# Kernel tuning notes

Hardware: AMD Instinct MI355X
Metric: run time of the kernel (lower is better)

## Reference

```python
import jax, jax.numpy as jnp
import numpy as np

NS, NW, E, DIN, OUT, H = 100_000, 400_000, 500_000, 64, 64, 4


def setup_inputs() -> dict:
    key = jax.random.key(0)
    ks = jax.random.split(key, 26)
    s = 1.0 / np.sqrt(DIN)
    sg = 1.0 / np.sqrt(OUT)
    inp = {
        "x_sites": jax.random.normal(ks[0], (NS, DIN), jnp.float32),
        "x_wells": jax.random.normal(ks[1], (NW, DIN), jnp.float32),
        "edge_sw_src": jax.random.randint(ks[2], (E,), 0, NS, jnp.int32),
        "edge_sw_dst": jax.random.randint(ks[3], (E,), 0, NW, jnp.int32),
        "edge_ws_src": jax.random.randint(ks[4], (E,), 0, NW, jnp.int32),
        "edge_ws_dst": jax.random.randint(ks[5], (E,), 0, NS, jnp.int32),
        # GAT ('pfas_sites','distance','gw_wells'), heads=4, concat=False
        "W_sw": jax.random.normal(ks[6], (DIN, H * OUT), jnp.float32) * s,
        "att_src_sw": jax.random.normal(ks[7], (H, OUT), jnp.float32) * sg,
        "att_dst_sw": jax.random.normal(ks[8], (H, OUT), jnp.float32) * sg,
        "b_sw": jnp.zeros((OUT,), jnp.float32),
        # SAGE ('gw_wells','distance','pfas_sites')
        "Wl_ws": jax.random.normal(ks[9], (DIN, OUT), jnp.float32) * s,
        "bl_ws": jnp.zeros((OUT,), jnp.float32),
        "Wr_ws": jax.random.normal(ks[10], (DIN, OUT), jnp.float32) * s,
        # GAT ('pfas_sites','self_loop','pfas_sites'), add_self_loops=True -> identity edges
        "W_ss": jax.random.normal(ks[11], (DIN, H * OUT), jnp.float32) * s,
        "att_src_ss": jax.random.normal(ks[12], (H, OUT), jnp.float32) * sg,
        "att_dst_ss": jax.random.normal(ks[13], (H, OUT), jnp.float32) * sg,
        "b_ss": jnp.zeros((OUT,), jnp.float32),
        # SAGE ('gw_wells','self_loop','gw_wells') with identity edges
        "Wl_ww": jax.random.normal(ks[14], (DIN, OUT), jnp.float32) * s,
        "bl_ww": jnp.zeros((OUT,), jnp.float32),
        "Wr_ww": jax.random.normal(ks[15], (DIN, OUT), jnp.float32) * s,
        # output heads
        "Wg": jax.random.normal(ks[16], (OUT, 1), jnp.float32) * sg,
        "bg": jnp.zeros((1,), jnp.float32),
        "Wsit": jax.random.normal(ks[17], (OUT, 1), jnp.float32) * sg,
        "bsit": jnp.zeros((1,), jnp.float32),
    }
    return inp


def _gat(x_src, x_dst, src, dst, W, a_src, a_dst, b, n_dst):
    """PyG GATConv, concat=False (mean over heads), negative_slope=0.2."""
    h, c = a_src.shape
    xs = (x_src @ W).reshape(-1, h, c)  # [Ns,H,C]
    xd = (x_dst @ W).reshape(-1, h, c)  # [Nd,H,C]
    al_s = jnp.einsum("nhc,hc->nh", xs, a_src)
    al_d = jnp.einsum("nhc,hc->nh", xd, a_dst)
    e = jax.nn.leaky_relu(al_s[src] + al_d[dst], 0.2)  # [E,H]
    m = jax.ops.segment_max(e, dst, num_segments=n_dst)
    ex = jnp.exp(e - m[dst])
    denom = jax.ops.segment_sum(ex, dst, num_segments=n_dst)
    alpha = ex / denom[dst]  # edge-softmax per dst node
    msg = xs[src] * alpha[:, :, None]  # [E,H,C] dominant intermediate
    out = jax.ops.segment_sum(msg, dst, num_segments=n_dst)
    return out.mean(axis=1) + b


def _sage(x_src, x_dst, src, dst, Wl, bl, Wr, n_dst):
    """PyG SAGEConv, mean aggregation, root_weight=True."""
    ssum = jax.ops.segment_sum(x_src[src], dst, num_segments=n_dst)
    cnt = jax.ops.segment_sum(jnp.ones((src.shape[0],), x_src.dtype), dst, num_segments=n_dst)
    mean = ssum / jnp.maximum(cnt, 1.0)[:, None]  # empty neighborhood -> 0 (PyG mean scatter)
    return mean @ Wl + bl + x_dst @ Wr


def reference(x_sites, x_wells, edge_sw_src, edge_sw_dst, edge_ws_src, edge_ws_dst,
              W_sw, att_src_sw, att_dst_sw, b_sw, Wl_ws, bl_ws, Wr_ws,
              W_ss, att_src_ss, att_dst_ss, b_ss, Wl_ww, bl_ww, Wr_ww,
              Wg, bg, Wsit, bsit):
    # relation 1: GAT sites -> wells
    gw = _gat(x_sites, x_wells, edge_sw_src, edge_sw_dst, W_sw, att_src_sw, att_dst_sw, b_sw, NW)
    # relation 4: SAGE self-loop on wells; identity edges -> mean == x itself
    gw = gw + (x_wells @ Wl_ww + bl_ww + x_wells @ Wr_ww)  # HeteroConv aggr='sum'
    # relation 2: SAGE wells -> sites
    si = _sage(x_wells, x_sites, edge_ws_src, edge_ws_dst, Wl_ws, bl_ws, Wr_ws, NS)
    # relation 3: GAT self-loop on sites (add_self_loops=True -> identity edge set);
    # softmax over a single self edge is 1, so output = mean over heads of lin(x) + bias
    si = si + (x_sites @ W_ss).reshape(NS, H, OUT).mean(axis=1) + b_ss
    # post: relu -> dropout (eval mode: identity) -> linear -> leaky_relu(0.01)
    gw = jax.nn.relu(gw)
    si = jax.nn.relu(si)
    o_gw = jax.nn.leaky_relu(gw @ Wg + bg, 0.01)   # [NW, 1]
    o_si = jax.nn.leaky_relu(si @ Wsit + bsit, 0.01)  # [NS, 1]
    return o_gw, o_si
```

## Files before the change

### kernel.cpp

```cpp
#include <hip/hip_runtime.h>

#define NS_ 100000
#define NW_ 400000
#define NE_ 500000
#define EPB 2048

typedef float f32x4_t __attribute__((ext_vector_type(4)));
typedef unsigned u32x4_t __attribute__((ext_vector_type(4)));

__device__ __forceinline__ float lrelu02(float x) { return x > 0.f ? x : 0.2f * x; }
__device__ __forceinline__ float bf2f(unsigned short u) {
    return __uint_as_float(((unsigned)u) << 16);
}
__device__ __forceinline__ unsigned short f2bf(float f) {
    unsigned u = __float_as_uint(f);
    u += 0x7FFFu + ((u >> 16) & 1u);
    return (unsigned short)(u >> 16);
}
__device__ __forceinline__ unsigned pk(float lo, float hi) {
    return (unsigned)f2bf(lo) | ((unsigned)f2bf(hi) << 16);
}
__device__ __forceinline__ void mfma_bf16(f32x4_t& acc, u32x4_t a, u32x4_t b) {
    asm volatile("v_mfma_f32_16x16x32_bf16 %0, %1, %2, %0" : "+v"(acc) : "v"(a), "v"(b));
}

__global__ void __launch_bounds__(256)
k_prep(const float* __restrict__ W_sw, const float* __restrict__ att_src,
       const float* __restrict__ att_dst,
       const float* __restrict__ Wl_ww, const float* __restrict__ Wr_ww,
       const float* __restrict__ Wl_ws, const float* __restrict__ Wr_ws,
       const float* __restrict__ W_ss,
       float* __restrict__ vd, float* __restrict__ vs,
       u32x4_t* __restrict__ fw, u32x4_t* __restrict__ fs,
       u32x4_t* __restrict__ fsp)
{
    const int tid = threadIdx.x;
    {
        int d = tid >> 2, h = tid & 3;
        const float4* wp = (const float4*)(W_sw + d * 256 + h * 64);
        const float4* ad = (const float4*)(att_dst + h * 64);
        const float4* as = (const float4*)(att_src + h * 64);
        float accd = 0.f, accs = 0.f;
#pragma unroll
        for (int c = 0; c < 16; ++c) {
            float4 wv = wp[c]; float4 dv = ad[c]; float4 sv = as[c];
            accd += wv.x * dv.x + wv.y * dv.y + wv.z * dv.z + wv.w * dv.w;
            accs += wv.x * sv.x + wv.y * sv.y + wv.z * sv.z + wv.w * sv.w;
        }
        vd[d * 4 + h] = accd;
        vs[d * 4 + h] = accs;
    }
    for (int idx = tid; idx < 512; idx += 256) {
        int f = idx >> 6, lane = idx & 63;
        int kc = f >> 2, ct = f & 3, q = lane >> 4, n = lane & 15;
        int c = ct * 16 + n;
        u32x4_t d;
#pragma unroll
        for (int i = 0; i < 4; ++i) {
            int k = kc * 32 + q * 8 + 2 * i;
            d[i] = pk(Wl_ww[k * 64 + c] + Wr_ww[k * 64 + c],
                      Wl_ww[(k + 1) * 64 + c] + Wr_ww[(k + 1) * 64 + c]);
        }
        fw[idx] = d;
    }
    for (int idx = tid; idx < 1024; idx += 256) {
        int f = idx >> 6, lane = idx & 63;
        int kc = f >> 2, ct = f & 3, q = lane >> 4, n = lane & 15;
        int c = ct * 16 + n;
        u32x4_t d;
#pragma unroll
        for (int i = 0; i < 4; ++i) {
            int k = kc * 32 + q * 8 + 2 * i;
            float lo, hi;
            if (k < 64) {
                lo = Wl_ws[k * 64 + c];
                hi = Wl_ws[(k + 1) * 64 + c];
            } else {
                int kk = k - 64;
                lo = Wr_ws[kk * 64 + c] + 0.25f * (W_ss[kk * 256 + c] + W_ss[kk * 256 + 64 + c] +
                                                   W_ss[kk * 256 + 128 + c] + W_ss[kk * 256 + 192 + c]);
                hi = Wr_ws[(kk + 1) * 64 + c] + 0.25f * (W_ss[(kk + 1) * 256 + c] + W_ss[(kk + 1) * 256 + 64 + c] +
                                                         W_ss[(kk + 1) * 256 + 128 + c] + W_ss[(kk + 1) * 256 + 192 + c]);
            }
            d[i] = pk(lo, hi);
        }
        fs[idx] = d;
    }
    for (int idx = tid; idx < 2048; idx += 256) {
        int f = idx >> 6, lane = idx & 63;
        int kc = f >> 4, ct = f & 15, q = lane >> 4, n = lane & 15;
        int c = ct * 16 + n;
        u32x4_t d;
#pragma unroll
        for (int i = 0; i < 4; ++i) {
            int k = kc * 32 + q * 8 + 2 * i;
            d[i] = pk(W_sw[k * 256 + c], W_sw[(k + 1) * 256 + c]);
        }
        fsp[idx] = d;
    }
}

#define SP_PAD 264
__global__ void __launch_bounds__(256)
k_sites_pre(const float* __restrict__ x_sites, const u32x4_t* __restrict__ fsp,
            const float* __restrict__ vs, unsigned short* __restrict__ xs,
            float* __restrict__ al_s)
{
    __shared__ unsigned short stg[4][16 * SP_PAD];
    __shared__ float vsl[256];
    const int tid = threadIdx.x;
    vsl[tid] = vs[tid];
    __syncthreads();
    const int wave = __builtin_amdgcn_readfirstlane(tid >> 6);
    const int lane = tid & 63, q = lane >> 4, n = lane & 15;
    const int sbase = blockIdx.x * 64 + wave * 16;
    const int srow = min(sbase + n, NS_ - 1);
    const float* xr = x_sites + (size_t)srow * 64 + q * 8;
    float4 x0 = *(const float4*)(xr);
    float4 x1 = *(const float4*)(xr + 4);
    float4 x2 = *(const float4*)(xr + 32);
    float4 x3 = *(const float4*)(xr + 36);
    u32x4_t am0 = { pk(x0.x, x0.y), pk(x0.z, x0.w), pk(x1.x, x1.y), pk(x1.z, x1.w) };
    u32x4_t am1 = { pk(x2.x, x2.y), pk(x2.z, x2.w), pk(x3.x, x3.y), pk(x3.z, x3.w) };
    float pa[4];
#pragma unroll
    for (int h = 0; h < 4; ++h) {
        const float* v0 = &vsl[(q * 8) * 4 + h];
        const float* v1 = &vsl[(32 + q * 8) * 4 + h];
        pa[h] = x0.x * v0[0]  + x0.y * v0[4]  + x0.z * v0[8]  + x0.w * v0[12]
              + x1.x * v0[16] + x1.y * v0[20] + x1.z * v0[24] + x1.w * v0[28]
              + x2.x * v1[0]  + x2.y * v1[4]  + x2.z * v1[8]  + x2.w * v1[12]
              + x3.x * v1[16] + x3.y * v1[20] + x3.z * v1[24] + x3.w * v1[28];
    }
#pragma unroll
    for (int h = 0; h < 4; ++h) {
        pa[h] += __shfl_xor(pa[h], 16, 64);
        pa[h] += __shfl_xor(pa[h], 32, 64);
    }
    if (q == 0 && sbase + n < NS_)
        *(float4*)(al_s + (size_t)(sbase + n) * 4) = make_float4(pa[0], pa[1], pa[2], pa[3]);

    f32x4_t acc[16];
#pragma unroll
    for (int ct = 0; ct < 16; ++ct) acc[ct] = (f32x4_t){0, 0, 0, 0};
    asm volatile("s_nop 3" : "+v"(am0), "+v"(am1));
#pragma unroll
    for (int ct = 0; ct < 16; ++ct) mfma_bf16(acc[ct], am0, fsp[ct * 64 + lane]);
#pragma unroll
    for (int ct = 0; ct < 16; ++ct) mfma_bf16(acc[ct], am1, fsp[(16 + ct) * 64 + lane]);
    asm volatile("s_nop 7\n\ts_nop 7" ::: "memory");
    unsigned short* ss = &stg[wave][0];
#pragma unroll
    for (int ct = 0; ct < 16; ++ct)
#pragma unroll
        for (int reg = 0; reg < 4; ++reg)
            ss[(q * 4 + reg) * SP_PAD + ct * 16 + n] = f2bf(acc[ct][reg]);
    __builtin_amdgcn_s_waitcnt(0);
#pragma unroll
    for (int i = 0; i < 8; ++i) {
        int g = i * 64 + lane;
        int r = g >> 5, c = g & 31;
        if (sbase + r < NS_) {
            u32x4_t v = *(const u32x4_t*)(ss + r * SP_PAD + c * 8);
            *(u32x4_t*)(xs + (size_t)(sbase + r) * 256 + c * 8) = v;
        }
    }
}

__global__ void __launch_bounds__(256)
k_hist2(const int* __restrict__ d1, int* __restrict__ h1,
        const int* __restrict__ d2, int* __restrict__ h2)
{
    int e = blockIdx.x * 256 + threadIdx.x;
    if (e >= NE_) return;
    if (blockIdx.y == 0) atomicAdd(&h1[d1[e]], 1);
    else                 atomicAdd(&h2[d2[e]], 1);
}

__global__ void __launch_bounds__(256)
k_scan1_2(const int* __restrict__ h1, int n1, int* __restrict__ b1, int nb1,
          const int* __restrict__ h2, int n2, int* __restrict__ b2)
{
    __shared__ int red[256];
    const int tid = threadIdx.x;
    const int bx = blockIdx.x;
    const int* hist; int n; int* bsum; int blk;
    if (bx < nb1) { hist = h1; n = n1; bsum = b1; blk = bx; }
    else          { hist = h2; n = n2; bsum = b2; blk = bx - nb1; }
    int base = blk * EPB + tid * 8;
    int s = 0;
#pragma unroll
    for (int i = 0; i < 8; ++i) { int idx = base + i; if (idx < n) s += hist[idx]; }
    red[tid] = s;
    __syncthreads();
    for (int off = 128; off > 0; off >>= 1) {
        if (tid < off) red[tid] += red[tid + off];
        __syncthreads();
    }
    if (tid == 0) bsum[blk] = red[0];
}

__global__ void __launch_bounds__(256)
k_scan2_2(int* __restrict__ b1, int nb1, int* __restrict__ b2, int nb2)
{
    __shared__ int sh[256];
    const int tid = threadIdx.x;
    int* bsum = blockIdx.x == 0 ? b1 : b2;
    int nb = blockIdx.x == 0 ? nb1 : nb2;
    sh[tid] = (tid < nb) ? bsum[tid] : 0;
    __syncthreads();
    for (int off = 1; off < 256; off <<= 1) {
        int u = (tid >= off) ? sh[tid - off] : 0;
        __syncthreads();
        sh[tid] += u;
        __syncthreads();
    }
    if (tid < nb) bsum[tid] = (tid == 0) ? 0 : sh[tid - 1];
}

__global__ void __launch_bounds__(256)
k_scan3_2(const int* __restrict__ h1, int n1, const int* __restrict__ b1,
          int* __restrict__ rp1, int* __restrict__ cu1, int nb1,
          const int* __restrict__ h2, int n2, const int* __restrict__ b2,
          int* __restrict__ rp2, int* __restrict__ cu2)
{
    __shared__ int tsum[256];
    const int tid = threadIdx.x;
    const int bx = blockIdx.x;
    const int* hist; int n; const int* bsum; int* rowptr; int* cursor; int blk;
    if (bx < nb1) { hist = h1; n = n1; bsum = b1; rowptr = rp1; cursor = cu1; blk = bx; }
    else          { hist = h2; n = n2; bsum = b2; rowptr = rp2; cursor = cu2; blk = bx - nb1; }
    int base = blk * EPB + tid * 8;
    int v[8]; int s = 0;
#pragma unroll
    for (int i = 0; i < 8; ++i) {
        int idx = base + i;
        v[i] = (idx < n) ? hist[idx] : 0;
        s += v[i];
    }
    tsum[tid] = s;
    __syncthreads();
    for (int off = 1; off < 256; off <<= 1) {
        int u = (tid >= off) ? tsum[tid - off] : 0;
        __syncthreads();
        tsum[tid] += u;
        __syncthreads();
    }
    int texcl = tsum[tid] - s;
    int run = bsum[blk] + texcl;
#pragma unroll
    for (int i = 0; i < 8; ++i) {
        int idx = base + i;
        if (idx < n) { rowptr[idx] = run; cursor[idx] = run; run += v[i]; }
    }
    if (blk == 0 && tid == 0) rowptr[n] = NE_;
}

__global__ void __launch_bounds__(256)
k_scatter2(const int* __restrict__ s1, const int* __restrict__ d1,
           int* __restrict__ c1, int* __restrict__ o1,
           const int* __restrict__ s2, const int* __restrict__ d2,
           int* __restrict__ c2, int* __restrict__ o2)
{
    int e = blockIdx.x * 256 + threadIdx.x;
    if (e >= NE_) return;
    if (blockIdx.y == 0) { int p = atomicAdd(&c1[d1[e]], 1); o1[p] = s1[e]; }
    else                 { int p = atomicAdd(&c2[d2[e]], 1); o2[p] = s2[e]; }
}

__global__ void __launch_bounds__(256)
k_gat_gather(const float* __restrict__ x_wells, const float* __restrict__ vd,
             const int* __restrict__ rowptr, const int* __restrict__ csr_src,
             const float* __restrict__ al_s, const unsigned short* __restrict__ xs,
             const float* __restrict__ b_sw, const float* __restrict__ bl_ww,
             unsigned short* __restrict__ tg)
{
    __shared__ float vdl[256];
    __shared__ float biasl[64];
    const int tid = threadIdx.x;
    vdl[tid] = vd[tid];
    if (tid < 64) biasl[tid] = b_sw[tid] + bl_ww[tid];
    __syncthreads();
    const int wl = tid >> 4, p = tid & 15;
    const int w = blockIdx.x * 16 + wl;
    float h0, h1, h2, h3;
    {
        float4 xv = *(const float4*)(x_wells + (size_t)w * 64 + 4 * p);
        const float* vp = &vdl[16 * p];
        h0 = xv.x * vp[0] + xv.y * vp[4] + xv.z * vp[8]  + xv.w * vp[12];
        h1 = xv.x * vp[1] + xv.y * vp[5] + xv.z * vp[9]  + xv.w * vp[13];
        h2 = xv.x * vp[2] + xv.y * vp[6] + xv.z * vp[10] + xv.w * vp[14];
        h3 = xv.x * vp[3] + xv.y * vp[7] + xv.z * vp[11] + xv.w * vp[15];
    }
#pragma unroll
    for (int off = 1; off < 16; off <<= 1) {
        h0 += __shfl_xor(h0, off, 64);
        h1 += __shfl_xor(h1, off, 64);
        h2 += __shfl_xor(h2, off, 64);
        h3 += __shfl_xor(h3, off, 64);
    }
    const int r0 = rowptr[w], r1 = rowptr[w + 1];
    float den0 = 0, den1 = 0, den2 = 0, den3 = 0;
    float n0[4] = {0, 0, 0, 0}, n1[4] = {0, 0, 0, 0};
    float n2[4] = {0, 0, 0, 0}, n3[4] = {0, 0, 0, 0};
    for (int j = r0; j < r1; ++j) {
        int s = csr_src[j];
        float4 as = ((const float4*)al_s)[s];
        float e0 = __expf(lrelu02(as.x + h0));
        float e1 = __expf(lrelu02(as.y + h1));
        float e2 = __expf(lrelu02(as.z + h2));
        float e3 = __expf(lrelu02(as.w + h3));
        den0 += e0; den1 += e1; den2 += e2; den3 += e3;
        const unsigned short* xr = xs + (size_t)s * 256 + 4 * p;
        ushort4 u0 = *(const ushort4*)(xr);
        ushort4 u1 = *(const ushort4*)(xr + 64);
        ushort4 u2 = *(const ushort4*)(xr + 128);
        ushort4 u3 = *(const ushort4*)(xr + 192);
        n0[0] += e0 * bf2f(u0.x); n0[1] += e0 * bf2f(u0.y); n0[2] += e0 * bf2f(u0.z); n0[3] += e0 * bf2f(u0.w);
        n1[0] += e1 * bf2f(u1.x); n1[1] += e1 * bf2f(u1.y); n1[2] += e1 * bf2f(u1.z); n1[3] += e1 * bf2f(u1.w);
        n2[0] += e2 * bf2f(u2.x); n2[1] += e2 * bf2f(u2.y); n2[2] += e2 * bf2f(u2.z); n2[3] += e2 * bf2f(u2.w);
        n3[0] += e3 * bf2f(u3.x); n3[1] += e3 * bf2f(u3.y); n3[2] += e3 * bf2f(u3.z); n3[3] += e3 * bf2f(u3.w);
    }
    const int c0 = 4 * p;
    float t[4];
    if (r1 > r0) {
        float i0 = 0.25f / den0, i1 = 0.25f / den1, i2 = 0.25f / den2, i3 = 0.25f / den3;
#pragma unroll
        for (int i = 0; i < 4; ++i)
            t[i] = n0[i] * i0 + n1[i] * i1 + n2[i] * i2 + n3[i] * i3 + biasl[c0 + i];
    } else {
#pragma unroll
        for (int i = 0; i < 4; ++i) t[i] = biasl[c0 + i];
    }
    ushort4 o;
    o.x = f2bf(t[0]); o.y = f2bf(t[1]); o.z = f2bf(t[2]); o.w = f2bf(t[3]);
    *(ushort4*)(tg + (size_t)w * 64 + c0) = o;
}

__global__ void __launch_bounds__(256)
k_wells_dense(const float* __restrict__ x_wells, const unsigned short* __restrict__ tg,
              const u32x4_t* __restrict__ fw, const float* __restrict__ Wg,
              const float* __restrict__ bg, float* __restrict__ out)
{
    const int tid = threadIdx.x;
    const int wave = __builtin_amdgcn_readfirstlane(tid >> 6);
    const int lane = tid & 63, q = lane >> 4, n = lane & 15;
    const int wbase = blockIdx.x * 64 + wave * 16;
    const float* xr = x_wells + (size_t)(wbase + n) * 64 + q * 8;
    float4 x0 = *(const float4*)(xr);
    float4 x1 = *(const float4*)(xr + 4);
    float4 x2 = *(const float4*)(xr + 32);
    float4 x3 = *(const float4*)(xr + 36);
    u32x4_t a0 = { pk(x0.x, x0.y), pk(x0.z, x0.w), pk(x1.x, x1.y), pk(x1.z, x1.w) };
    u32x4_t a1 = { pk(x2.x, x2.y), pk(x2.z, x2.w), pk(x3.x, x3.y), pk(x3.z, x3.w) };
    f32x4_t acc0 = {0, 0, 0, 0}, acc1 = {0, 0, 0, 0}, acc2 = {0, 0, 0, 0}, acc3 = {0, 0, 0, 0};
    asm volatile("s_nop 3" : "+v"(a0), "+v"(a1), "+v"(acc0), "+v"(acc1), "+v"(acc2), "+v"(acc3));
    mfma_bf16(acc0, a0, fw[0 * 64 + lane]);
    mfma_bf16(acc1, a0, fw[1 * 64 + lane]);
    mfma_bf16(acc2, a0, fw[2 * 64 + lane]);
    mfma_bf16(acc3, a0, fw[3 * 64 + lane]);
    mfma_bf16(acc0, a1, fw[4 * 64 + lane]);
    mfma_bf16(acc1, a1, fw[5 * 64 + lane]);
    mfma_bf16(acc2, a1, fw[6 * 64 + lane]);
    mfma_bf16(acc3, a1, fw[7 * 64 + lane]);
    asm volatile("s_nop 7\n\ts_nop 7" : "+v"(acc0), "+v"(acc1), "+v"(acc2), "+v"(acc3));
    const float wg0 = Wg[n], wg1 = Wg[16 + n], wg2 = Wg[32 + n], wg3 = Wg[48 + n];
    const float bg0 = bg[0];
    float pr[4];
#pragma unroll
    for (int reg = 0; reg < 4; ++reg) {
        const int w = wbase + q * 4 + reg;
        const unsigned short* tr = tg + (size_t)w * 64 + n;
        float t0 = acc0[reg] + bf2f(tr[0]);
        float t1 = acc1[reg] + bf2f(tr[16]);
        float t2 = acc2[reg] + bf2f(tr[32]);
        float t3 = acc3[reg] + bf2f(tr[48]);
        float p = fmaxf(t0, 0.f) * wg0 + fmaxf(t1, 0.f) * wg1 +
                  fmaxf(t2, 0.f) * wg2 + fmaxf(t3, 0.f) * wg3;
        p += __shfl_xor(p, 1, 64);
        p += __shfl_xor(p, 2, 64);
        p += __shfl_xor(p, 4, 64);
        p += __shfl_xor(p, 8, 64);
        pr[reg] = p + bg0;
    }
    if (n == 0) {
        float4 o;
        o.x = pr[0] > 0.f ? pr[0] : 0.01f * pr[0];
        o.y = pr[1] > 0.f ? pr[1] : 0.01f * pr[1];
        o.z = pr[2] > 0.f ? pr[2] : 0.01f * pr[2];
        o.w = pr[3] > 0.f ? pr[3] : 0.01f * pr[3];
        *(float4*)(out + wbase + q * 4) = o;
    }
}

__global__ void __launch_bounds__(256)
k_sage_gather(const float* __restrict__ x_wells, const int* __restrict__ rowptr,
              const int* __restrict__ csr_src, unsigned short* __restrict__ mn)
{
    const int tid = threadIdx.x;
    const int sl = tid >> 4, p = tid & 15;
    const int s = blockIdx.x * 16 + sl;
    const int r0 = rowptr[s], r1 = rowptr[s + 1];
    float4 acc = {0.f, 0.f, 0.f, 0.f};
    for (int j = r0; j < r1; ++j) {
        int wsrc = csr_src[j];
        float4 xv = ((const float4*)(x_wells + (size_t)wsrc * 64))[p];
        acc.x += xv.x; acc.y += xv.y; acc.z += xv.z; acc.w += xv.w;
    }
    if (r1 > r0) {
        float rc = 1.f / (float)(r1 - r0);
        acc.x *= rc; acc.y *= rc; acc.z *= rc; acc.w *= rc;
    }
    ushort4 o;
    o.x = f2bf(acc.x); o.y = f2bf(acc.y); o.z = f2bf(acc.z); o.w = f2bf(acc.w);
    *(ushort4*)(mn + (size_t)s * 64 + 4 * p) = o;
}

__global__ void __launch_bounds__(256)
k_sites_dense(const float* __restrict__ x_sites, const unsigned short* __restrict__ mn,
              const u32x4_t* __restrict__ fs, const float* __restrict__ bl_ws,
              const float* __restrict__ b_ss, const float* __restrict__ Wsit,
              const float* __restrict__ bsit, float* __restrict__ out)
{
    const int tid = threadIdx.x;
    const int wave = __builtin_amdgcn_readfirstlane(tid >> 6);
    const int lane = tid & 63, q = lane >> 4, n = lane & 15;
    const int sbase = blockIdx.x * 64 + wave * 16;
    const int srow = min(sbase + n, NS_ - 1);
    u32x4_t am0 = *(const u32x4_t*)(mn + (size_t)srow * 64 + q * 8);
    u32x4_t am1 = *(const u32x4_t*)(mn + (size_t)srow * 64 + 32 + q * 8);
    const float* xr = x_sites + (size_t)srow * 64 + q * 8;
    float4 x0 = *(const float4*)(xr);
    float4 x1 = *(const float4*)(xr + 4);
    float4 x2 = *(const float4*)(xr + 32);
    float4 x3 = *(const float4*)(xr + 36);
    u32x4_t ax0 = { pk(x0.x, x0.y), pk(x0.z, x0.w), pk(x1.x, x1.y), pk(x1.z, x1.w) };
    u32x4_t ax1 = { pk(x2.x, x2.y), pk(x2.z, x2.w), pk(x3.x, x3.y), pk(x3.z, x3.w) };
    f32x4_t acc0 = {0, 0, 0, 0}, acc1 = {0, 0, 0, 0}, acc2 = {0, 0, 0, 0}, acc3 = {0, 0, 0, 0};
    asm volatile("s_nop 3" : "+v"(ax0), "+v"(ax1), "+v"(acc0), "+v"(acc1), "+v"(acc2), "+v"(acc3));
    mfma_bf16(acc0, am0, fs[0 * 64 + lane]);
    mfma_bf16(acc1, am0, fs[1 * 64 + lane]);
    mfma_bf16(acc2, am0, fs[2 * 64 + lane]);
    mfma_bf16(acc3, am0, fs[3 * 64 + lane]);
    mfma_bf16(acc0, am1, fs[4 * 64 + lane]);
    mfma_bf16(acc1, am1, fs[5 * 64 + lane]);
    mfma_bf16(acc2, am1, fs[6 * 64 + lane]);
    mfma_bf16(acc3, am1, fs[7 * 64 + lane]);
    mfma_bf16(acc0, ax0, fs[8 * 64 + lane]);
    mfma_bf16(acc1, ax0, fs[9 * 64 + lane]);
    mfma_bf16(acc2, ax0, fs[10 * 64 + lane]);
    mfma_bf16(acc3, ax0, fs[11 * 64 + lane]);
    mfma_bf16(acc0, ax1, fs[12 * 64 + lane]);
    mfma_bf16(acc1, ax1, fs[13 * 64 + lane]);
    mfma_bf16(acc2, ax1, fs[14 * 64 + lane]);
    mfma_bf16(acc3, ax1, fs[15 * 64 + lane]);
    asm volatile("s_nop 7\n\ts_nop 7" : "+v"(acc0), "+v"(acc1), "+v"(acc2), "+v"(acc3));
    const float b0 = bl_ws[n] + b_ss[n];
    const float b1 = bl_ws[16 + n] + b_ss[16 + n];
    const float b2 = bl_ws[32 + n] + b_ss[32 + n];
    const float b3 = bl_ws[48 + n] + b_ss[48 + n];
    const float w0 = Wsit[n], w1 = Wsit[16 + n], w2 = Wsit[32 + n], w3 = Wsit[48 + n];
    const float bs0 = bsit[0];
    float pr[4];
#pragma unroll
    for (int reg = 0; reg < 4; ++reg) {
        float t0 = acc0[reg] + b0;
        float t1 = acc1[reg] + b1;
        float t2 = acc2[reg] + b2;
        float t3 = acc3[reg] + b3;
        float p = fmaxf(t0, 0.f) * w0 + fmaxf(t1, 0.f) * w1 +
                  fmaxf(t2, 0.f) * w2 + fmaxf(t3, 0.f) * w3;
        p += __shfl_xor(p, 1, 64);
        p += __shfl_xor(p, 2, 64);
        p += __shfl_xor(p, 4, 64);
        p += __shfl_xor(p, 8, 64);
        pr[reg] = p + bs0;
    }
    if (n == 0) {
        const int s4 = sbase + q * 4;
        if (s4 + 3 < NS_) {
            float4 o;
            o.x = pr[0] > 0.f ? pr[0] : 0.01f * pr[0];
            o.y = pr[1] > 0.f ? pr[1] : 0.01f * pr[1];
            o.z = pr[2] > 0.f ? pr[2] : 0.01f * pr[2];
            o.w = pr[3] > 0.f ? pr[3] : 0.01f * pr[3];
            *(float4*)(out + (size_t)NW_ + s4) = o;
        } else {
#pragma unroll
            for (int reg = 0; reg < 4; ++reg) {
                if (s4 + reg < NS_) {
                    float v = pr[reg];
                    out[(size_t)NW_ + s4 + reg] = v > 0.f ? v : 0.01f * v;
                }
            }
        }
    }
}

extern "C" void kernel_launch(void* const* d_in, const int* in_sizes, int n_in,
                              void* d_out, int out_size, void* d_ws, size_t ws_size,
                              hipStream_t stream)
{
    const float* x_sites    = (const float*)d_in[0];
    const float* x_wells    = (const float*)d_in[1];
    const int*   e_sw_src   = (const int*)d_in[2];
    const int*   e_sw_dst   = (const int*)d_in[3];
    const int*   e_ws_src   = (const int*)d_in[4];
    const int*   e_ws_dst   = (const int*)d_in[5];
    const float* W_sw       = (const float*)d_in[6];
    const float* att_src_sw = (const float*)d_in[7];
    const float* att_dst_sw = (const float*)d_in[8];
    const float* b_sw       = (const float*)d_in[9];
    const float* Wl_ws      = (const float*)d_in[10];
    const float* bl_ws      = (const float*)d_in[11];
    const float* Wr_ws      = (const float*)d_in[12];
    const float* W_ss       = (const float*)d_in[13];
    const float* b_ss       = (const float*)d_in[16];
    const float* Wl_ww      = (const float*)d_in[17];
    const float* bl_ww      = (const float*)d_in[18];
    const float* Wr_ww      = (const float*)d_in[19];
    const float* Wg         = (const float*)d_in[20];
    const float* bg         = (const float*)d_in[21];
    const float* Wsit       = (const float*)d_in[22];
    const float* bsit       = (const float*)d_in[23];
    float* out = (float*)d_out;

    unsigned short* xs = (unsigned short*)d_ws;
    unsigned short* tg = xs + (size_t)NS_ * 256;
    unsigned short* mn = tg + (size_t)NW_ * 64;
    float* al_s = (float*)(mn + (size_t)NS_ * 64);
    float* vd   = al_s + (size_t)NS_ * 4;
    float* vs   = vd + 256;
    u32x4_t* fw = (u32x4_t*)(vs + 256);
    u32x4_t* fs = fw + 512;
    u32x4_t* fsp= fs + 1024;
    int* ip     = (int*)(fsp + 2048);
    int* h_sw   = ip;
    int* h_ws   = h_sw + NW_;
    int* rp_sw  = h_ws + NS_;
    int* cur_sw = rp_sw + NW_ + 4;
    int* csr_sw = cur_sw + NW_;
    int* bs_sw  = csr_sw + NE_;
    int* rp_ws  = bs_sw + 256;
    int* cur_ws = rp_ws + NS_ + 4;
    int* csr_ws = cur_ws + NS_;
    int* bs_ws  = csr_ws + NE_;

    hipMemsetAsync(h_sw, 0, (size_t)(NW_ + NS_) * sizeof(int), stream);

    const int egrid = (NE_ + 255) / 256;
    const int nb_sw = (NW_ + EPB - 1) / EPB;
    const int nb_ws = (NS_ + EPB - 1) / EPB;

    hipLaunchKernelGGL(k_hist2, dim3(egrid, 2), dim3(256), 0, stream,
                       e_sw_dst, h_sw, e_ws_dst, h_ws);
    hipLaunchKernelGGL(k_scan1_2, dim3(nb_sw + nb_ws), dim3(256), 0, stream,
                       h_sw, NW_, bs_sw, nb_sw, h_ws, NS_, bs_ws);
    hipLaunchKernelGGL(k_scan2_2, dim3(2), dim3(256), 0, stream,
                       bs_sw, nb_sw, bs_ws, nb_ws);
    hipLaunchKernelGGL(k_scan3_2, dim3(nb_sw + nb_ws), dim3(256), 0, stream,
                       h_sw, NW_, bs_sw, rp_sw, cur_sw, nb_sw,
                       h_ws, NS_, bs_ws, rp_ws, cur_ws);
    hipLaunchKernelGGL(k_scatter2, dim3(egrid, 2), dim3(256), 0, stream,
                       e_sw_src, e_sw_dst, cur_sw, csr_sw,
                       e_ws_src, e_ws_dst, cur_ws, csr_ws);

    hipLaunchKernelGGL(k_prep, dim3(1), dim3(256), 0, stream,
                       W_sw, att_src_sw, att_dst_sw, Wl_ww, Wr_ww, Wl_ws, Wr_ws, W_ss,
                       vd, vs, fw, fs, fsp);
    hipLaunchKernelGGL(k_sites_pre, dim3((NS_ + 63) / 64), dim3(256), 0, stream,
                       x_sites, fsp, vs, xs, al_s);

    hipLaunchKernelGGL(k_gat_gather, dim3(NW_ / 16), dim3(256), 0, stream,
                       x_wells, vd, rp_sw, csr_sw, al_s, xs, b_sw, bl_ww, tg);
    hipLaunchKernelGGL(k_wells_dense, dim3(NW_ / 64), dim3(256), 0, stream,
                       x_wells, tg, fw, Wg, bg, out);
    hipLaunchKernelGGL(k_sage_gather, dim3(NS_ / 16), dim3(256), 0, stream,
                       x_wells, rp_ws, csr_ws, mn);
    hipLaunchKernelGGL(k_sites_dense, dim3((NS_ + 63) / 64), dim3(256), 0, stream,
                       x_sites, mn, fs, bl_ws, b_ss, Wsit, bsit, out);
}
```

Baseline: 492.7 us.

## Fuse gather and dense MFMA stages for wells and sites into single kernels

Merges the GAT gather with the wells dense projection and head, and the SAGE mean gather with the sites dense projection and head, into two kernels. Intermediate bf16 buffers (tg, mn) no longer round-trip through global memory, and the data is staged in shared memory instead. Each 16-row block now splits the 64 output columns across its four waves with one MFMA chain each. This cuts two launches and intermediate traffic, but adds block-level syncs and LDS pressure inside the gather kernels, which may lower occupancy.

Result: faster. 468.5 us (-4.9%).

```diff
diff --git a/kernel.cpp b/kernel.cpp
--- a/kernel.cpp
+++ b/kernel.cpp
@@ -269,24 +269,30 @@
 }
 
 __global__ void __launch_bounds__(256)
-k_gat_gather(const float* __restrict__ x_wells, const float* __restrict__ vd,
-             const int* __restrict__ rowptr, const int* __restrict__ csr_src,
-             const float* __restrict__ al_s, const unsigned short* __restrict__ xs,
-             const float* __restrict__ b_sw, const float* __restrict__ bl_ww,
-             unsigned short* __restrict__ tg)
-{
-    __shared__ float vdl[256];
+k_gat_wells(const float* __restrict__ x_wells, const float* __restrict__ vd,
+            const int* __restrict__ rowptr, const int* __restrict__ csr_src,
+            const float* __restrict__ al_s, const unsigned short* __restrict__ xs,
+            const float* __restrict__ b_sw, const float* __restrict__ bl_ww,
+            const u32x4_t* __restrict__ fw, const float* __restrict__ Wg,
+            const float* __restrict__ bg, float* __restrict__ out)
+{
+    __shared__ float vdl[16][17];
+    __shared__ float xw[16][68];
+    __shared__ float dl[16][68];
     __shared__ float biasl[64];
-    const int tid = threadIdx.x;
-    vdl[tid] = vd[tid];
-    if (tid < 64) biasl[tid] = b_sw[tid] + bl_ww[tid];
+    __shared__ float wgl[64];
+    __shared__ float res[16];
+    const int tid = threadIdx.x;
+    vdl[tid >> 4][tid & 15] = vd[tid];
+    if (tid < 64) { biasl[tid] = b_sw[tid] + bl_ww[tid]; wgl[tid] = Wg[tid]; }
     __syncthreads();
     const int wl = tid >> 4, p = tid & 15;
     const int w = blockIdx.x * 16 + wl;
     float h0, h1, h2, h3;
     {
         float4 xv = *(const float4*)(x_wells + (size_t)w * 64 + 4 * p);
-        const float* vp = &vdl[16 * p];
+        *(float4*)&xw[wl][4 * p] = xv;
+        const float* vp = vdl[p];
         h0 = xv.x * vp[0] + xv.y * vp[4] + xv.z * vp[8]  + xv.w * vp[12];
         h1 = xv.x * vp[1] + xv.y * vp[5] + xv.z * vp[9]  + xv.w * vp[13];
         h2 = xv.x * vp[2] + xv.y * vp[6] + xv.z * vp[10] + xv.w * vp[14];
@@ -322,178 +328,125 @@
         n3[0] += e3 * bf2f(u3.x); n3[1] += e3 * bf2f(u3.y); n3[2] += e3 * bf2f(u3.z); n3[3] += e3 * bf2f(u3.w);
     }
     const int c0 = 4 * p;
-    float t[4];
+    float tmsg[4];
     if (r1 > r0) {
         float i0 = 0.25f / den0, i1 = 0.25f / den1, i2 = 0.25f / den2, i3 = 0.25f / den3;
 #pragma unroll
         for (int i = 0; i < 4; ++i)
-            t[i] = n0[i] * i0 + n1[i] * i1 + n2[i] * i2 + n3[i] * i3 + biasl[c0 + i];
+            tmsg[i] = n0[i] * i0 + n1[i] * i1 + n2[i] * i2 + n3[i] * i3 + biasl[c0 + i];
     } else {
 #pragma unroll
-        for (int i = 0; i < 4; ++i) t[i] = biasl[c0 + i];
-    }
-    ushort4 o;
-    o.x = f2bf(t[0]); o.y = f2bf(t[1]); o.z = f2bf(t[2]); o.w = f2bf(t[3]);
-    *(ushort4*)(tg + (size_t)w * 64 + c0) = o;
-}
-
-__global__ void __launch_bounds__(256)
-k_wells_dense(const float* __restrict__ x_wells, const unsigned short* __restrict__ tg,
-              const u32x4_t* __restrict__ fw, const float* __restrict__ Wg,
-              const float* __restrict__ bg, float* __restrict__ out)
-{
-    const int tid = threadIdx.x;
+        for (int i = 0; i < 4; ++i) tmsg[i] = biasl[c0 + i];
+    }
+    __syncthreads();
     const int wave = __builtin_amdgcn_readfirstlane(tid >> 6);
     const int lane = tid & 63, q = lane >> 4, n = lane & 15;
-    const int wbase = blockIdx.x * 64 + wave * 16;
-    const float* xr = x_wells + (size_t)(wbase + n) * 64 + q * 8;
-    float4 x0 = *(const float4*)(xr);
-    float4 x1 = *(const float4*)(xr + 4);
-    float4 x2 = *(const float4*)(xr + 32);
-    float4 x3 = *(const float4*)(xr + 36);
-    u32x4_t a0 = { pk(x0.x, x0.y), pk(x0.z, x0.w), pk(x1.x, x1.y), pk(x1.z, x1.w) };
-    u32x4_t a1 = { pk(x2.x, x2.y), pk(x2.z, x2.w), pk(x3.x, x3.y), pk(x3.z, x3.w) };
-    f32x4_t acc0 = {0, 0, 0, 0}, acc1 = {0, 0, 0, 0}, acc2 = {0, 0, 0, 0}, acc3 = {0, 0, 0, 0};
-    asm volatile("s_nop 3" : "+v"(a0), "+v"(a1), "+v"(acc0), "+v"(acc1), "+v"(acc2), "+v"(acc3));
-    mfma_bf16(acc0, a0, fw[0 * 64 + lane]);
-    mfma_bf16(acc1, a0, fw[1 * 64 + lane]);
-    mfma_bf16(acc2, a0, fw[2 * 64 + lane]);
-    mfma_bf16(acc3, a0, fw[3 * 64 + lane]);
-    mfma_bf16(acc0, a1, fw[4 * 64 + lane]);
-    mfma_bf16(acc1, a1, fw[5 * 64 + lane]);
-    mfma_bf16(acc2, a1, fw[6 * 64 + lane]);
-    mfma_bf16(acc3, a1, fw[7 * 64 + lane]);
-    asm volatile("s_nop 7\n\ts_nop 7" : "+v"(acc0), "+v"(acc1), "+v"(acc2), "+v"(acc3));
-    const float wg0 = Wg[n], wg1 = Wg[16 + n], wg2 = Wg[32 + n], wg3 = Wg[48 + n];
-    const float bg0 = bg[0];
-    float pr[4];
-#pragma unroll
-    for (int reg = 0; reg < 4; ++reg) {
-        const int w = wbase + q * 4 + reg;
-        const unsigned short* tr = tg + (size_t)w * 64 + n;
-        float t0 = acc0[reg] + bf2f(tr[0]);
-        float t1 = acc1[reg] + bf2f(tr[16]);
-        float t2 = acc2[reg] + bf2f(tr[32]);
-        float t3 = acc3[reg] + bf2f(tr[48]);
-        float p = fmaxf(t0, 0.f) * wg0 + fmaxf(t1, 0.f) * wg1 +
-                  fmaxf(t2, 0.f) * wg2 + fmaxf(t3, 0.f) * wg3;
-        p += __shfl_xor(p, 1, 64);
-        p += __shfl_xor(p, 2, 64);
-        p += __shfl_xor(p, 4, 64);
-        p += __shfl_xor(p, 8, 64);
-        pr[reg] = p + bg0;
-    }
-    if (n == 0) {
-        float4 o;
-        o.x = pr[0] > 0.f ? pr[0] : 0.01f * pr[0];
-        o.y = pr[1] > 0.f ? pr[1] : 0.01f * pr[1];
-        o.z = pr[2] > 0.f ? pr[2] : 0.01f * pr[2];
-        o.w = pr[3] > 0.f ? pr[3] : 0.01f * pr[3];
-        *(float4*)(out + wbase + q * 4) = o;
-    }
-}
-
-__global__ void __launch_bounds__(256)
-k_sage_gather(const float* __restrict__ x_wells, const int* __restrict__ rowptr,
-              const int* __restrict__ csr_src, unsigned short* __restrict__ mn)
-{
-    const int tid = threadIdx.x;
+    u32x4_t a0, a1;
+#pragma unroll
+    for (int i = 0; i < 4; ++i) {
+        a0[i] = pk(xw[n][q * 8 + 2 * i],      xw[n][q * 8 + 2 * i + 1]);
+        a1[i] = pk(xw[n][32 + q * 8 + 2 * i], xw[n][32 + q * 8 + 2 * i + 1]);
+    }
+    f32x4_t acc = {0, 0, 0, 0};
+    asm volatile("s_nop 3" : "+v"(a0), "+v"(a1), "+v"(acc));
+    mfma_bf16(acc, a0, fw[wave * 64 + lane]);
+    mfma_bf16(acc, a1, fw[(4 + wave) * 64 + lane]);
+    asm volatile("s_nop 7\n\ts_nop 7" : "+v"(acc));
+#pragma unroll
+    for (int reg = 0; reg < 4; ++reg)
+        dl[q * 4 + reg][wave * 16 + n] = acc[reg];
+    __syncthreads();
+    float4 dv = *(const float4*)&dl[wl][c0];
+    float t0 = tmsg[0] + dv.x;
+    float t1 = tmsg[1] + dv.y;
+    float t2 = tmsg[2] + dv.z;
+    float t3 = tmsg[3] + dv.w;
+    float pr = fmaxf(t0, 0.f) * wgl[c0] + fmaxf(t1, 0.f) * wgl[c0 + 1] +
+               fmaxf(t2, 0.f) * wgl[c0 + 2] + fmaxf(t3, 0.f) * wgl[c0 + 3];
+    pr += __shfl_xor(pr, 1, 64);
+    pr += __shfl_xor(pr, 2, 64);
+    pr += __shfl_xor(pr, 4, 64);
+    pr += __shfl_xor(pr, 8, 64);
+    if (p == 0) res[wl] = pr + bg[0];
+    __syncthreads();
+    if (tid < 16) {
+        float v = res[tid];
+        out[blockIdx.x * 16 + tid] = v > 0.f ? v : 0.01f * v;
+    }
+}
+
+__global__ void __launch_bounds__(256)
+k_sage_sites(const float* __restrict__ x_sites, const float* __restrict__ x_wells,
+             const int* __restrict__ rowptr, const int* __restrict__ csr_src,
+             const u32x4_t* __restrict__ fs, const float* __restrict__ bl_ws,
+             const float* __restrict__ b_ss, const float* __restrict__ Wsit,
+             const float* __restrict__ bsit, float* __restrict__ out)
+{
+    __shared__ float mnL[16][68];
+    __shared__ float xL[16][68];
+    __shared__ float dl[16][68];
+    __shared__ float biasl[64];
+    __shared__ float wsl[64];
+    __shared__ float res[16];
+    const int tid = threadIdx.x;
+    if (tid < 64) { biasl[tid] = bl_ws[tid] + b_ss[tid]; wsl[tid] = Wsit[tid]; }
     const int sl = tid >> 4, p = tid & 15;
     const int s = blockIdx.x * 16 + sl;
     const int r0 = rowptr[s], r1 = rowptr[s + 1];
-    float4 acc = {0.f, 0.f, 0.f, 0.f};
+    float4 m4 = {0.f, 0.f, 0.f, 0.f};
     for (int j = r0; j < r1; ++j) {
         int wsrc = csr_src[j];
         float4 xv = ((const float4*)(x_wells + (size_t)wsrc * 64))[p];
-        acc.x += xv.x; acc.y += xv.y; acc.z += xv.z; acc.w += xv.w;
+        m4.x += xv.x; m4.y += xv.y; m4.z += xv.z; m4.w += xv.w;
     }
     if (r1 > r0) {
         float rc = 1.f / (float)(r1 - r0);
-        acc.x *= rc; acc.y *= rc; acc.z *= rc; acc.w *= rc;
-    }
-    ushort4 o;
-    o.x = f2bf(acc.x); o.y = f2bf(acc.y); o.z = f2bf(acc.z); o.w = f2bf(acc.w);
-    *(ushort4*)(mn + (size_t)s * 64 + 4 * p) = o;
-}
-
-__global__ void __launch_bounds__(256)
-k_sites_dense(const float* __restrict__ x_sites, const unsigned short* __restrict__ mn,
-              const u32x4_t* __restrict__ fs, const float* __restrict__ bl_ws,
-              const float* __restrict__ b_ss, const float* __restrict__ Wsit,
-              const float* __restrict__ bsit, float* __restrict__ out)
-{
-    const int tid = threadIdx.x;
+        m4.x *= rc; m4.y *= rc; m4.z *= rc; m4.w *= rc;
+    }
+    *(float4*)&mnL[sl][4 * p] = m4;
+    {
+        float4 xv = *(const float4*)(x_sites + (size_t)s * 64 + 4 * p);
+        *(float4*)&xL[sl][4 * p] = xv;
+    }
+    __syncthreads();
     const int wave = __builtin_amdgcn_readfirstlane(tid >> 6);
     const int lane = tid & 63, q = lane >> 4, n = lane & 15;
-    const int sbase = blockIdx.x * 64 + wave * 16;
-    const int srow = min(sbase + n, NS_ - 1);
-    u32x4_t am0 = *(const u32x4_t*)(mn + (size_t)srow * 64 + q * 8);
-    u32x4_t am1 = *(const u32x4_t*)(mn + (size_t)srow * 64 + 32 + q * 8);
-    const float* xr = x_sites + (size_t)srow * 64 + q * 8;
-    float4 x0 = *(const float4*)(xr);
-    float4 x1 = *(const float4*)(xr + 4);
-    float4 x2 = *(const float4*)(xr + 32);
-    float4 x3 = *(const float4*)(xr + 36);
-    u32x4_t ax0 = { pk(x0.x, x0.y), pk(x0.z, x0.w), pk(x1.x, x1.y), pk(x1.z, x1.w) };
-    u32x4_t ax1 = { pk(x2.x, x2.y), pk(x2.z, x2.w), pk(x3.x, x3.y), pk(x3.z, x3.w) };
-    f32x4_t acc0 = {0, 0, 0, 0}, acc1 = {0, 0, 0, 0}, acc2 = {0, 0, 0, 0}, acc3 = {0, 0, 0, 0};
-    asm volatile("s_nop 3" : "+v"(ax0), "+v"(ax1), "+v"(acc0), "+v"(acc1), "+v"(acc2), "+v"(acc3));
-    mfma_bf16(acc0, am0, fs[0 * 64 + lane]);
-    mfma_bf16(acc1, am0, fs[1 * 64 + lane]);
-    mfma_bf16(acc2, am0, fs[2 * 64 + lane]);
-    mfma_bf16(acc3, am0, fs[3 * 64 + lane]);
-    mfma_bf16(acc0, am1, fs[4 * 64 + lane]);
-    mfma_bf16(acc1, am1, fs[5 * 64 + lane]);
-    mfma_bf16(acc2, am1, fs[6 * 64 + lane]);
-    mfma_bf16(acc3, am1, fs[7 * 64 + lane]);
-    mfma_bf16(acc0, ax0, fs[8 * 64 + lane]);
-    mfma_bf16(acc1, ax0, fs[9 * 64 + lane]);
-    mfma_bf16(acc2, ax0, fs[10 * 64 + lane]);
-    mfma_bf16(acc3, ax0, fs[11 * 64 + lane]);
-    mfma_bf16(acc0, ax1, fs[12 * 64 + lane]);
-    mfma_bf16(acc1, ax1, fs[13 * 64 + lane]);
-    mfma_bf16(acc2, ax1, fs[14 * 64 + lane]);
-    mfma_bf16(acc3, ax1, fs[15 * 64 + lane]);
-    asm volatile("s_nop 7\n\ts_nop 7" : "+v"(acc0), "+v"(acc1), "+v"(acc2), "+v"(acc3));
-    const float b0 = bl_ws[n] + b_ss[n];
-    const float b1 = bl_ws[16 + n] + b_ss[16 + n];
-    const float b2 = bl_ws[32 + n] + b_ss[32 + n];
-    const float b3 = bl_ws[48 + n] + b_ss[48 + n];
-    const float w0 = Wsit[n], w1 = Wsit[16 + n], w2 = Wsit[32 + n], w3 = Wsit[48 + n];
-    const float bs0 = bsit[0];
-    float pr[4];
-#pragma unroll
-    for (int reg = 0; reg < 4; ++reg) {
-        float t0 = acc0[reg] + b0;
-        float t1 = acc1[reg] + b1;
-        float t2 = acc2[reg] + b2;
-        float t3 = acc3[reg] + b3;
-        float p = fmaxf(t0, 0.f) * w0 + fmaxf(t1, 0.f) * w1 +
-                  fmaxf(t2, 0.f) * w2 + fmaxf(t3, 0.f) * w3;
-        p += __shfl_xor(p, 1, 64);
-        p += __shfl_xor(p, 2, 64);
-        p += __shfl_xor(p, 4, 64);
-        p += __shfl_xor(p, 8, 64);
-        pr[reg] = p + bs0;
-    }
-    if (n == 0) {
-        const int s4 = sbase + q * 4;
-        if (s4 + 3 < NS_) {
-            float4 o;
-            o.x = pr[0] > 0.f ? pr[0] : 0.01f * pr[0];
-            o.y = pr[1] > 0.f ? pr[1] : 0.01f * pr[1];
-            o.z = pr[2] > 0.f ? pr[2] : 0.01f * pr[2];
-            o.w = pr[3] > 0.f ? pr[3] : 0.01f * pr[3];
-            *(float4*)(out + (size_t)NW_ + s4) = o;
-        } else {
-#pragma unroll
-            for (int reg = 0; reg < 4; ++reg) {
-                if (s4 + reg < NS_) {
-                    float v = pr[reg];
-                    out[(size_t)NW_ + s4 + reg] = v > 0.f ? v : 0.01f * v;
-                }
-            }
-        }
+    u32x4_t am0, am1, ax0, ax1;
+#pragma unroll
+    for (int i = 0; i < 4; ++i) {
+        am0[i] = pk(mnL[n][q * 8 + 2 * i],      mnL[n][q * 8 + 2 * i + 1]);
+        am1[i] = pk(mnL[n][32 + q * 8 + 2 * i], mnL[n][32 + q * 8 + 2 * i + 1]);
+        ax0[i] = pk(xL[n][q * 8 + 2 * i],       xL[n][q * 8 + 2 * i + 1]);
+        ax1[i] = pk(xL[n][32 + q * 8 + 2 * i],  xL[n][32 + q * 8 + 2 * i + 1]);
+    }
+    f32x4_t acc = {0, 0, 0, 0};
+    asm volatile("s_nop 3" : "+v"(am0), "+v"(am1), "+v"(ax0), "+v"(ax1), "+v"(acc));
+    mfma_bf16(acc, am0, fs[wave * 64 + lane]);
+    mfma_bf16(acc, am1, fs[(4 + wave) * 64 + lane]);
+    mfma_bf16(acc, ax0, fs[(8 + wave) * 64 + lane]);
+    mfma_bf16(acc, ax1, fs[(12 + wave) * 64 + lane]);
+    asm volatile("s_nop 7\n\ts_nop 7" : "+v"(acc));
+#pragma unroll
+    for (int reg = 0; reg < 4; ++reg)
+        dl[q * 4 + reg][wave * 16 + n] = acc[reg];
+    __syncthreads();
+    const int c0 = 4 * p;
+    float4 dv = *(const float4*)&dl[sl][c0];
+    float t0 = dv.x + biasl[c0];
+    float t1 = dv.y + biasl[c0 + 1];
+    float t2 = dv.z + biasl[c0 + 2];
+    float t3 = dv.w + biasl[c0 + 3];
+    float pr = fmaxf(t0, 0.f) * wsl[c0] + fmaxf(t1, 0.f) * wsl[c0 + 1] +
+               fmaxf(t2, 0.f) * wsl[c0 + 2] + fmaxf(t3, 0.f) * wsl[c0 + 3];
+    pr += __shfl_xor(pr, 1, 64);
+    pr += __shfl_xor(pr, 2, 64);
+    pr += __shfl_xor(pr, 4, 64);
+    pr += __shfl_xor(pr, 8, 64);
+    if (p == 0) res[sl] = pr + bsit[0];
+    __syncthreads();
+    if (tid < 16) {
+        float v = res[tid];
+        out[(size_t)NW_ + blockIdx.x * 16 + tid] = v > 0.f ? v : 0.01f * v;
     }
 }
 
@@ -526,9 +479,7 @@
     float* out = (float*)d_out;
 
     unsigned short* xs = (unsigned short*)d_ws;
-    unsigned short* tg = xs + (size_t)NS_ * 256;
-    unsigned short* mn = tg + (size_t)NW_ * 64;
-    float* al_s = (float*)(mn + (size_t)NS_ * 64);
+    float* al_s = (float*)(xs + (size_t)NS_ * 256);
     float* vd   = al_s + (size_t)NS_ * 4;
     float* vs   = vd + 256;
     u32x4_t* fw = (u32x4_t*)(vs + 256);
@@ -571,12 +522,10 @@
     hipLaunchKernelGGL(k_sites_pre, dim3((NS_ + 63) / 64), dim3(256), 0, stream,
                        x_sites, fsp, vs, xs, al_s);
 
-    hipLaunchKernelGGL(k_gat_gather, dim3(NW_ / 16), dim3(256), 0, stream,
-                       x_wells, vd, rp_sw, csr_sw, al_s, xs, b_sw, bl_ww, tg);
-    hipLaunchKernelGGL(k_wells_dense, dim3(NW_ / 64), dim3(256), 0, stream,
-                       x_wells, tg, fw, Wg, bg, out);
-    hipLaunchKernelGGL(k_sage_gather, dim3(NS_ / 16), dim3(256), 0, stream,
-                       x_wells, rp_ws, csr_ws, mn);
-    hipLaunchKernelGGL(k_sites_dense, dim3((NS_ + 63) / 64), dim3(256), 0, stream,
-                       x_sites, mn, fs, bl_ws, b_ss, Wsit, bsit, out);
-}
+    hipLaunchKernelGGL(k_gat_wells, dim3(NW_ / 16), dim3(256), 0, stream,
+                       x_wells, vd, rp_sw, csr_sw, al_s, xs, b_sw, bl_ww,
+                       fw, Wg, bg, out);
+    hipLaunchKernelGGL(k_sage_sites, dim3(NS_ / 16), dim3(256), 0, stream,
+                       x_sites, x_wells, rp_ws, csr_ws, fs, bl_ws, b_ss,
+                       Wsit, bsit, out);
+}
```
